# Kernel tuning notes

Hardware: AMD Instinct MI355X
Metric: run time of the kernel (lower is better)

## Reference

```python
import jax, jax.numpy as jnp
import numpy as np

NEG_SLOPE = 0.2  # PyG GATConv default


def gat_layer(x, src, dst, W, a_src, a_dst, b, num_nodes):
    """Single-head GATConv (heads=1, add_self_loops handled by caller)."""
    xw = x @ W  # [N, H]
    s_src = xw @ a_src  # [N] per-node source attention logits
    s_dst = xw @ a_dst  # [N]
    e = jax.nn.leaky_relu(s_src[src] + s_dst[dst], NEG_SLOPE)  # [E]
    # segment softmax over incoming edges of each dst node
    m = jax.ops.segment_max(e, dst, num_segments=num_nodes)  # [N]
    ex = jnp.exp(e - m[dst])
    denom = jax.ops.segment_sum(ex, dst, num_segments=num_nodes)  # [N]
    alpha = ex / denom[dst]  # [E]
    out = jax.ops.segment_sum(alpha[:, None] * xw[src], dst, num_segments=num_nodes)
    return out + b


def setup_inputs() -> dict:
    key = jax.random.key(0)
    N, F_IN, H, E, B = 100000, 256, 64, 1000000, 16384
    ks = jax.random.split(key, 16)
    s = lambda fan: 1.0 / np.sqrt(fan)
    return {
        "x": jax.random.normal(ks[0], (N, F_IN), dtype=jnp.float32),
        "edge_index": jax.random.randint(ks[1], (2, E), 0, N, dtype=jnp.int64),
        "user_indices": jax.random.randint(ks[2], (B,), 0, N, dtype=jnp.int64),
        "movie_indices": jax.random.randint(ks[3], (B,), 0, N, dtype=jnp.int64),
        "W1": jax.random.normal(ks[4], (F_IN, H), dtype=jnp.float32) * s(F_IN),
        "a_src1": jax.random.normal(ks[5], (H,), dtype=jnp.float32) * s(H),
        "a_dst1": jax.random.normal(ks[6], (H,), dtype=jnp.float32) * s(H),
        "b1": jnp.zeros((H,), dtype=jnp.float32),
        "W2": jax.random.normal(ks[7], (H, H), dtype=jnp.float32) * s(H),
        "a_src2": jax.random.normal(ks[8], (H,), dtype=jnp.float32) * s(H),
        "a_dst2": jax.random.normal(ks[9], (H,), dtype=jnp.float32) * s(H),
        "b2": jnp.zeros((H,), dtype=jnp.float32),
        "fc_W": jax.random.normal(ks[10], (2 * H, 1), dtype=jnp.float32) * s(2 * H),
        "fc_b": jnp.zeros((1,), dtype=jnp.float32),
    }


def reference(x, edge_index, user_indices, movie_indices,
              W1, a_src1, a_dst1, b1, W2, a_src2, a_dst2, b2, fc_W, fc_b):
    N = x.shape[0]
    # PyG GATConv default add_self_loops=True: append (i, i) edges
    loops = jnp.arange(N, dtype=edge_index.dtype)
    src = jnp.concatenate([edge_index[0], loops])
    dst = jnp.concatenate([edge_index[1], loops])
    h = gat_layer(x, src, dst, W1, a_src1, a_dst1, b1, N)
    h = jax.nn.relu(h)
    h = gat_layer(h, src, dst, W2, a_src2, a_dst2, b2, N)
    combined = jnp.concatenate([h[user_indices], h[movie_indices]], axis=1)  # [B, 2H]
    return combined @ fc_W + fc_b  # [B, 1]
```

## Files before the change

### kernel.cpp

```cpp
#include <hip/hip_runtime.h>
#include <hip/hip_bf16.h>
#include <hip/hip_fp16.h>

#define LRELU_SLOPE 0.2f
#define CSR_STRIDE 32

__device__ __forceinline__ float lrelu(float x) { return x > 0.f ? x : LRELU_SLOPE * x; }

typedef __attribute__((ext_vector_type(8))) short short8;
typedef __attribute__((ext_vector_type(4))) float f32x4;

__device__ __forceinline__ unsigned short f2bf(float f) {
    unsigned u = __builtin_bit_cast(unsigned, f);
    u = (u + 0x7FFFu + ((u >> 16) & 1u)) >> 16;
    return (unsigned short)u;
}
__device__ __forceinline__ float bf2f(unsigned short b) {
    unsigned u = ((unsigned)b) << 16;
    return __builtin_bit_cast(float, u);
}

template <int K>
__device__ __forceinline__ void packW_body(const float* __restrict__ W,
                                           unsigned short* __restrict__ Bhi,
                                           unsigned short* __restrict__ Blo,
                                           int blk, int t) {
    constexpr int NKC = K / 32;
    int g = blk * 256 + t;
    if (g >= 4 * NKC * 64) return;
    int lane = g & 63;
    int kc = (g >> 6) % NKC;
    int ct = g / (64 * NKC);
    int qd = lane >> 4, col = lane & 15;
    #pragma unroll
    for (int j = 0; j < 8; j++) {
        int k = kc * 32 + qd * 8 + j;
        float w = W[(size_t)k * 64 + ct * 16 + col];
        unsigned short h = f2bf(w);
        float rem = w - bf2f(h);
        Bhi[(size_t)g * 8 + j] = h;
        Blo[(size_t)g * 8 + j] = f2bf(rem);
    }
}

__global__ __launch_bounds__(256) void k_prep(const float* __restrict__ W1,
                                              unsigned short* __restrict__ b1hi, unsigned short* __restrict__ b1lo,
                                              const float* __restrict__ W2,
                                              unsigned short* __restrict__ b2hi, unsigned short* __restrict__ b2lo,
                                              int* __restrict__ deg, int* __restrict__ ovfCnt, int N) {
    int b = blockIdx.x;
    if (b < 8)  { packW_body<256>(W1, b1hi, b1lo, b, threadIdx.x); return; }
    if (b < 10) { packW_body<64>(W2, b2hi, b2lo, b - 8, threadIdx.x); return; }
    int i = (b - 10) * 256 + threadIdx.x;
    if (i < N) deg[i] = 0;
    if (i == 0) *ovfCnt = 0;
}

__global__ void k_build(const int* __restrict__ src, const int* __restrict__ dst,
                        int* __restrict__ deg, int* __restrict__ csr,
                        int* __restrict__ ovfCnt, int2* __restrict__ ovf, int E) {
    int i = (blockIdx.x * blockDim.x + threadIdx.x) * 4;
    if (i + 3 < E) {
        int4 d4 = *(const int4*)(dst + i);
        int4 s4 = *(const int4*)(src + i);
        int p0 = atomicAdd(&deg[d4.x], 1);
        int p1 = atomicAdd(&deg[d4.y], 1);
        int p2 = atomicAdd(&deg[d4.z], 1);
        int p3 = atomicAdd(&deg[d4.w], 1);
        if (p0 < CSR_STRIDE) csr[d4.x * CSR_STRIDE + p0] = s4.x;
        else { int o = atomicAdd(ovfCnt, 1); ovf[o] = make_int2(d4.x, s4.x); }
        if (p1 < CSR_STRIDE) csr[d4.y * CSR_STRIDE + p1] = s4.y;
        else { int o = atomicAdd(ovfCnt, 1); ovf[o] = make_int2(d4.y, s4.y); }
        if (p2 < CSR_STRIDE) csr[d4.z * CSR_STRIDE + p2] = s4.z;
        else { int o = atomicAdd(ovfCnt, 1); ovf[o] = make_int2(d4.z, s4.z); }
        if (p3 < CSR_STRIDE) csr[d4.w * CSR_STRIDE + p3] = s4.w;
        else { int o = atomicAdd(ovfCnt, 1); ovf[o] = make_int2(d4.w, s4.w); }
    } else {
        for (int j = i; j < E; j++) {
            int d = dst[j], s = src[j];
            int p = atomicAdd(&deg[d], 1);
            if (p < CSR_STRIDE) csr[d * CSR_STRIDE + p] = s;
            else { int o = atomicAdd(ovfCnt, 1); ovf[o] = make_int2(d, s); }
        }
    }
}

template <int K>
__device__ __forceinline__ void mfma_body(const float* __restrict__ X,
                                          const unsigned short* __restrict__ Bhi,
                                          const unsigned short* __restrict__ Blo,
                                          const float* __restrict__ a_s, const float* __restrict__ a_d,
                                          __half* __restrict__ XW, float* __restrict__ Ssrc,
                                          float* __restrict__ Sdst, int N, int blk) {
    constexpr int NKC = K / 32;
    int t = threadIdx.x, lane = t & 63, wid = t >> 6;
    int mtile = blk * 4 + wid;
    if (mtile * 16 >= N) return;
    int m0 = mtile * 16;
    int qd = lane >> 4, col = lane & 15;

    int rA = m0 + col;
    rA = rA < N ? rA : N - 1;
    const float* xrow = X + (size_t)rA * K + qd * 8;

    const short8* bh = (const short8*)Bhi;
    const short8* bl = (const short8*)Blo;

    f32x4 acc[4];
    #pragma unroll
    for (int ct = 0; ct < 4; ct++) acc[ct] = (f32x4){0.f, 0.f, 0.f, 0.f};

    #pragma clang loop unroll(disable)
    for (int kc = 0; kc < NKC; kc++) {
        const float* xp = xrow + kc * 32;
        float4 xa = *(const float4*)xp;
        float4 xb = *(const float4*)(xp + 4);
        float xv[8] = {xa.x, xa.y, xa.z, xa.w, xb.x, xb.y, xb.z, xb.w};
        short8 ah, al;
        #pragma unroll
        for (int j = 0; j < 8; j++) {
            unsigned short h = f2bf(xv[j]);
            ah[j] = (short)h;
            al[j] = (short)f2bf(xv[j] - bf2f(h));
        }
        #pragma unroll
        for (int ct = 0; ct < 4; ct++) {
            short8 wh = bh[(ct * NKC + kc) * 64 + lane];
            short8 wl = bl[(ct * NKC + kc) * 64 + lane];
            acc[ct] = __builtin_amdgcn_mfma_f32_16x16x32_bf16(ah, wh, acc[ct], 0, 0, 0);
            acc[ct] = __builtin_amdgcn_mfma_f32_16x16x32_bf16(al, wh, acc[ct], 0, 0, 0);
            acc[ct] = __builtin_amdgcn_mfma_f32_16x16x32_bf16(ah, wl, acc[ct], 0, 0, 0);
        }
    }

    float asx[4], adx[4];
    #pragma unroll
    for (int ct = 0; ct < 4; ct++) {
        asx[ct] = a_s[ct * 16 + col];
        adx[ct] = a_d[ct * 16 + col];
    }
    #pragma unroll
    for (int r = 0; r < 4; r++) {
        int row = m0 + qd * 4 + r;
        if (row < N) {
            float vs = 0.f, vd = 0.f;
            #pragma unroll
            for (int ct = 0; ct < 4; ct++) {
                float v = acc[ct][r];
                XW[(size_t)row * 64 + ct * 16 + col] = __float2half(v);
                vs += v * asx[ct];
                vd += v * adx[ct];
            }
            #pragma unroll
            for (int d = 1; d < 16; d <<= 1) {
                vs += __shfl_xor(vs, d);
                vd += __shfl_xor(vd, d);
            }
            if (col == 0) { Ssrc[row] = vs; Sdst[row] = vd; }
        }
    }
}

template <int K>
__global__ __launch_bounds__(256) void k_mfma(const float* __restrict__ X,
                                              const unsigned short* __restrict__ Bhi,
                                              const unsigned short* __restrict__ Blo,
                                              const float* __restrict__ a_s, const float* __restrict__ a_d,
                                              __half* __restrict__ XW, float* __restrict__ Ssrc,
                                              float* __restrict__ Sdst, int N) {
    mfma_body<K>(X, Bhi, Blo, a_s, a_d, XW, Ssrc, Sdst, N, blockIdx.x);
}

__global__ __launch_bounds__(256) void k_attn(const __half* __restrict__ XW, const float* __restrict__ Ssrc,
                                              const float* __restrict__ Sdst, const int* __restrict__ csr,
                                              const int* __restrict__ deg,
                                              const int* __restrict__ ovfCnt, const int2* __restrict__ ovf,
                                              const float* __restrict__ bias, float* __restrict__ H,
                                              int N, int do_relu) {
    int t = threadIdx.x, lane = t & 63, wid = t >> 6;
    int q = lane >> 4;
    int c = lane & 15;
    int n = (blockIdx.x * 4 + wid) * 4 + q;
    bool valid = n < N;
    int nc = valid ? n : N - 1;

    int d = deg[nc];
    int st = nc * CSR_STRIDE;
    float sd = Sdst[nc];
    int d32 = d < CSR_STRIDE ? d : CSR_STRIDE;
    int dcap = d < 16 ? d : 16;

    int myS = 0;
    if (c < dcap) myS = csr[st + c];

    int s0 = __shfl(myS, q * 16 + 0), s1 = __shfl(myS, q * 16 + 1);
    int s2 = __shfl(myS, q * 16 + 2), s3 = __shfl(myS, q * 16 + 3);
    float2 rs = *(const float2*)(XW + (size_t)nc * 64 + c * 4);
    float2 r0 = *(const float2*)(XW + (size_t)s0 * 64 + c * 4);
    float2 r1 = *(const float2*)(XW + (size_t)s1 * 64 + c * 4);
    float2 r2 = *(const float2*)(XW + (size_t)s2 * 64 + c * 4);
    float2 r3 = *(const float2*)(XW + (size_t)s3 * 64 + c * 4);

    float wself = __expf(lrelu(Ssrc[nc] + sd));
    float myW = 0.f;
    if (c < dcap) myW = __expf(lrelu(Ssrc[myS] + sd));
    float dpart = myW + ((c == 0) ? wself : 0.f);

    float4 acc4 = make_float4(0.f, 0.f, 0.f, 0.f);
    auto accum = [&](float2 raw, float w) {
        const __half2* hp = (const __half2*)&raw;
        float2 f0 = __half22float2(hp[0]);
        float2 f1 = __half22float2(hp[1]);
        acc4.x += w * f0.x; acc4.y += w * f0.y; acc4.z += w * f1.x; acc4.w += w * f1.y;
    };

    float w0 = __shfl(myW, q * 16 + 0), w1 = __shfl(myW, q * 16 + 1);
    float w2 = __shfl(myW, q * 16 + 2), w3 = __shfl(myW, q * 16 + 3);
    accum(rs, wself);
    accum(r0, w0); accum(r1, w1); accum(r2, w2); accum(r3, w3);

    for (int i = 4; i < dcap; i += 4) {
        int t0 = __shfl(myS, q * 16 + i + 0), t1 = __shfl(myS, q * 16 + i + 1);
        int t2 = __shfl(myS, q * 16 + i + 2), t3 = __shfl(myS, q * 16 + i + 3);
        float2 q0 = *(const float2*)(XW + (size_t)t0 * 64 + c * 4);
        float2 q1 = *(const float2*)(XW + (size_t)t1 * 64 + c * 4);
        float2 q2 = *(const float2*)(XW + (size_t)t2 * 64 + c * 4);
        float2 q3 = *(const float2*)(XW + (size_t)t3 * 64 + c * 4);
        float v0 = __shfl(myW, q * 16 + i + 0), v1 = __shfl(myW, q * 16 + i + 1);
        float v2 = __shfl(myW, q * 16 + i + 2), v3 = __shfl(myW, q * 16 + i + 3);
        accum(q0, v0); accum(q1, v1); accum(q2, v2); accum(q3, v3);
    }

    for (int i = 16; i < d32; i++) {
        int s = csr[st + i];
        float w = __expf(lrelu(Ssrc[s] + sd));
        if (c == 0) dpart += w;
        float2 qv = *(const float2*)(XW + (size_t)s * 64 + c * 4);
        accum(qv, w);
    }

    int nov = *ovfCnt;
    if (nov > 0) {
        for (int j = 0; j < nov; j++) {
            int2 e = ovf[j];
            if (e.x == nc) {
                float w = __expf(lrelu(Ssrc[e.y] + sd));
                if (c == 0) dpart += w;
                float2 qv = *(const float2*)(XW + (size_t)e.y * 64 + c * 4);
                accum(qv, w);
            }
        }
    }

    #pragma unroll
    for (int dd = 8; dd > 0; dd >>= 1) dpart += __shfl_xor(dpart, dd);

    if (valid) {
        float4 b4 = *(const float4*)&bias[c * 4];
        float inv = 1.f / dpart;
        float4 o;
        o.x = acc4.x * inv + b4.x;
        o.y = acc4.y * inv + b4.y;
        o.z = acc4.z * inv + b4.z;
        o.w = acc4.w * inv + b4.w;
        if (do_relu) {
            o.x = fmaxf(o.x, 0.f); o.y = fmaxf(o.y, 0.f);
            o.z = fmaxf(o.z, 0.f); o.w = fmaxf(o.w, 0.f);
        }
        *(float4*)&H[(size_t)n * 64 + c * 4] = o;
    }
}

__global__ __launch_bounds__(256) void k_head(const float* __restrict__ H, const int* __restrict__ ui,
                                              const int* __restrict__ mi, const float* __restrict__ fcW,
                                              const float* __restrict__ fcb, float* __restrict__ out, int B) {
    int t = threadIdx.x, lane = t & 63, wid = t >> 6;
    int i = blockIdx.x * 4 + wid;
    if (i >= B) return;
    int u = ui[i], m = mi[i];
    float v = H[(size_t)u * 64 + lane] * fcW[lane] + H[(size_t)m * 64 + lane] * fcW[64 + lane];
    #pragma unroll
    for (int dd = 32; dd > 0; dd >>= 1) v += __shfl_xor(v, dd);
    if (lane == 0) out[i] = v + fcb[0];
}

extern "C" void kernel_launch(void* const* d_in, const int* in_sizes, int n_in,
                              void* d_out, int out_size, void* d_ws, size_t ws_size,
                              hipStream_t stream) {
    const float* x   = (const float*)d_in[0];
    const int*   ei  = (const int*)d_in[1];
    const int*   ui  = (const int*)d_in[2];
    const int*   mi  = (const int*)d_in[3];
    const float* W1  = (const float*)d_in[4];
    const float* as1 = (const float*)d_in[5];
    const float* ad1 = (const float*)d_in[6];
    const float* b1  = (const float*)d_in[7];
    const float* W2  = (const float*)d_in[8];
    const float* as2 = (const float*)d_in[9];
    const float* ad2 = (const float*)d_in[10];
    const float* b2  = (const float*)d_in[11];
    const float* fcW = (const float*)d_in[12];
    const float* fcb = (const float*)d_in[13];
    float* out = (float*)d_out;

    const int Hdim = in_sizes[5];
    const int FIN  = in_sizes[4] / Hdim;
    const int N    = in_sizes[0] / FIN;
    const int E    = in_sizes[1] / 2;
    const int B    = in_sizes[2];

    char* w = (char*)d_ws;
    auto alloc = [&](size_t bytes) -> void* {
        void* p = (void*)w;
        w += (bytes + 255) & ~(size_t)255;
        return p;
    };
    __half* xw  = (__half*)alloc((size_t)N * 64 * 2);
    float* hbuf = (float*)alloc((size_t)N * 64 * 4);
    float* ssrc = (float*)alloc((size_t)N * 4);
    float* sdst = (float*)alloc((size_t)N * 4);
    int* deg    = (int*)alloc((size_t)N * 4);
    int* csr    = (int*)alloc((size_t)N * CSR_STRIDE * 4);
    int* ovfCnt = (int*)alloc(256);
    int2* ovf   = (int2*)alloc((size_t)65536 * 8);
    unsigned short* b1hi = (unsigned short*)alloc((size_t)4 * 8 * 64 * 8 * 2);
    unsigned short* b1lo = (unsigned short*)alloc((size_t)4 * 8 * 64 * 8 * 2);
    unsigned short* b2hi = (unsigned short*)alloc((size_t)4 * 2 * 64 * 8 * 2);
    unsigned short* b2lo = (unsigned short*)alloc((size_t)4 * 2 * 64 * 8 * 2);

    const int* esrc = ei;
    const int* edst = ei + E;

    const int mfmaBlocks = ((N + 15) / 16 + 3) / 4;
    const int attnBlocks = (N + 15) / 16;

    int prepBlocks = 10 + (N + 255) / 256;
    k_prep<<<prepBlocks, 256, 0, stream>>>(W1, b1hi, b1lo, W2, b2hi, b2lo, deg, ovfCnt, N);

    k_build<<<(E / 4 + 255) / 256, 256, 0, stream>>>(esrc, edst, deg, csr, ovfCnt, ovf, E);

    k_mfma<256><<<mfmaBlocks, 256, 0, stream>>>(x, b1hi, b1lo, as1, ad1, xw, ssrc, sdst, N);
    k_attn<<<attnBlocks, 256, 0, stream>>>(xw, ssrc, sdst, csr, deg, ovfCnt, ovf, b1, hbuf, N, 1);

    k_mfma<64><<<mfmaBlocks, 256, 0, stream>>>(hbuf, b2hi, b2lo, as2, ad2, xw, ssrc, sdst, N);
    k_attn<<<attnBlocks, 256, 0, stream>>>(xw, ssrc, sdst, csr, deg, ovfCnt, ovf, b2, hbuf, N, 0);

    k_head<<<(B + 3) / 4, 256, 0, stream>>>(hbuf, ui, mi, fcW, fcb, out, B);
}
```

Before: 335.0 us.

## Compute second GAT layer aggregation only for queried user and movie nodes

```diff
diff --git a/kernel.cpp b/kernel.cpp
--- a/kernel.cpp
+++ b/kernel.cpp
@@ -47,13 +47,38 @@
                                               unsigned short* __restrict__ b1hi, unsigned short* __restrict__ b1lo,
                                               const float* __restrict__ W2,
                                               unsigned short* __restrict__ b2hi, unsigned short* __restrict__ b2lo,
-                                              int* __restrict__ deg, int* __restrict__ ovfCnt, int N) {
+                                              int* __restrict__ deg, int* __restrict__ flags,
+                                              int* __restrict__ misc, int N) {
     int b = blockIdx.x;
     if (b < 8)  { packW_body<256>(W1, b1hi, b1lo, b, threadIdx.x); return; }
     if (b < 10) { packW_body<64>(W2, b2hi, b2lo, b - 8, threadIdx.x); return; }
     int i = (b - 10) * 256 + threadIdx.x;
-    if (i < N) deg[i] = 0;
-    if (i == 0) *ovfCnt = 0;
+    if (i < N) { deg[i] = 0; flags[i] = 0; }
+    if (i == 0) { misc[0] = 0; misc[1] = 0; }
+}
+
+__global__ void k_mark(const int* __restrict__ ui, const int* __restrict__ mi,
+                       int* __restrict__ flags, int B) {
+    int i = blockIdx.x * blockDim.x + threadIdx.x;
+    if (i < B) { flags[ui[i]] = 1; flags[mi[i]] = 1; }
+}
+
+__global__ __launch_bounds__(256) void k_compact(const int* __restrict__ flags, int* __restrict__ list,
+                                                 int* __restrict__ cnt, int N) {
+    int idx = blockIdx.x * 256 + threadIdx.x;
+    int lane = threadIdx.x & 63;
+    int v = (idx < N) ? flags[idx] : 0;
+    int incl = v;
+    #pragma unroll
+    for (int d = 1; d < 64; d <<= 1) {
+        int u = __shfl_up(incl, d);
+        if (lane >= d) incl += u;
+    }
+    int total = __shfl(incl, 63);
+    int base = 0;
+    if (lane == 0) base = atomicAdd(cnt, total);
+    base = __shfl(base, 0);
+    if (idx < N && v) list[base + incl - 1] = idx;
 }
 
 __global__ void k_build(const int* __restrict__ src, const int* __restrict__ dst,
@@ -175,14 +200,24 @@
                                               const float* __restrict__ Sdst, const int* __restrict__ csr,
                                               const int* __restrict__ deg,
                                               const int* __restrict__ ovfCnt, const int2* __restrict__ ovf,
+                                              const int* __restrict__ list, const int* __restrict__ cntp,
                                               const float* __restrict__ bias, float* __restrict__ H,
                                               int N, int do_relu) {
     int t = threadIdx.x, lane = t & 63, wid = t >> 6;
     int q = lane >> 4;
     int c = lane & 15;
-    int n = (blockIdx.x * 4 + wid) * 4 + q;
-    bool valid = n < N;
-    int nc = valid ? n : N - 1;
+    int i4 = (blockIdx.x * 4 + wid) * 4 + q;
+    bool valid;
+    int n;
+    if (list) {
+        int cnt = *cntp;
+        valid = i4 < cnt;
+        n = valid ? list[i4] : 0;
+    } else {
+        valid = i4 < N;
+        n = valid ? i4 : 0;
+    }
+    int nc = n;
 
     int d = deg[nc];
     int st = nc * CSR_STRIDE;
@@ -320,8 +355,10 @@
     float* ssrc = (float*)alloc((size_t)N * 4);
     float* sdst = (float*)alloc((size_t)N * 4);
     int* deg    = (int*)alloc((size_t)N * 4);
+    int* flags  = (int*)alloc((size_t)N * 4);
+    int* list   = (int*)alloc((size_t)2 * B * 4);
     int* csr    = (int*)alloc((size_t)N * CSR_STRIDE * 4);
-    int* ovfCnt = (int*)alloc(256);
+    int* misc   = (int*)alloc(256);
     int2* ovf   = (int2*)alloc((size_t)65536 * 8);
     unsigned short* b1hi = (unsigned short*)alloc((size_t)4 * 8 * 64 * 8 * 2);
     unsigned short* b1lo = (unsigned short*)alloc((size_t)4 * 8 * 64 * 8 * 2);
@@ -330,20 +367,28 @@
 
     const int* esrc = ei;
     const int* edst = ei + E;
+    int* ovfCnt = misc;
+    int* listCnt = misc + 1;
 
     const int mfmaBlocks = ((N + 15) / 16 + 3) / 4;
     const int attnBlocks = (N + 15) / 16;
+    const int attn2Blocks = (2 * B + 15) / 16;
 
     int prepBlocks = 10 + (N + 255) / 256;
-    k_prep<<<prepBlocks, 256, 0, stream>>>(W1, b1hi, b1lo, W2, b2hi, b2lo, deg, ovfCnt, N);
+    k_prep<<<prepBlocks, 256, 0, stream>>>(W1, b1hi, b1lo, W2, b2hi, b2lo, deg, flags, misc, N);
+
+    k_mark<<<(B + 255) / 256, 256, 0, stream>>>(ui, mi, flags, B);
+    k_compact<<<(N + 255) / 256, 256, 0, stream>>>(flags, list, listCnt, N);
 
     k_build<<<(E / 4 + 255) / 256, 256, 0, stream>>>(esrc, edst, deg, csr, ovfCnt, ovf, E);
 
     k_mfma<256><<<mfmaBlocks, 256, 0, stream>>>(x, b1hi, b1lo, as1, ad1, xw, ssrc, sdst, N);
-    k_attn<<<attnBlocks, 256, 0, stream>>>(xw, ssrc, sdst, csr, deg, ovfCnt, ovf, b1, hbuf, N, 1);
+    k_attn<<<attnBlocks, 256, 0, stream>>>(xw, ssrc, sdst, csr, deg, ovfCnt, ovf,
+                                           (const int*)nullptr, (const int*)nullptr, b1, hbuf, N, 1);
 
     k_mfma<64><<<mfmaBlocks, 256, 0, stream>>>(hbuf, b2hi, b2lo, as2, ad2, xw, ssrc, sdst, N);
-    k_attn<<<attnBlocks, 256, 0, stream>>>(xw, ssrc, sdst, csr, deg, ovfCnt, ovf, b2, hbuf, N, 0);
+    k_attn<<<attn2Blocks, 256, 0, stream>>>(xw, ssrc, sdst, csr, deg, ovfCnt, ovf,
+                                            list, listCnt, b2, hbuf, N, 0);
 
     k_head<<<(B + 3) / 4, 256, 0, stream>>>(hbuf, ui, mi, fcW, fcb, out, B);
 }
```

After: 350.9 us. 4.7% more time.
